# Kernel optimization log

Measured on AMD Instinct MI355X. Metric: run time of the kernel, lower is better.

Reference implementation:

```python
import jax, jax.numpy as jnp
import numpy as np


def setup_inputs() -> dict:
    key = jax.random.key(0)
    k1, k2, k3 = jax.random.split(key, 3)
    B, C, W, H, K = 8, 3, 512, 512, 13
    Wo, Ho = W - K + 1, H - K + 1
    return {
        "img": jax.random.normal(k1, (B, C, W, H), dtype=jnp.float32),
        "hori": jax.random.normal(k2, (B, K, Wo, Ho), dtype=jnp.float32),
        "vert": jax.random.normal(k3, (B, K, Wo, Ho), dtype=jnp.float32),
        "kernel_size": K,
    }


def reference(img, hori, vert, kernel_size):
    # out[b,c,i,j] = sum_{u,v} img[b,c,i+u,j+v] * vert[b,u,i,j] * hori[b,v,i,j]
    K = kernel_size
    B, C, W, H = img.shape
    Wo, Ho = W - K + 1, H - K + 1
    out = jnp.zeros((B, C, Wo, Ho), img.dtype)
    # Fixed small K x K loop over kernel taps; all pixel/batch dims vectorized.
    for v in range(K):
        h_v = hori[:, v][:, None]  # [B,1,Wo,Ho]
        acc = jnp.zeros((B, C, Wo, Ho), img.dtype)
        for u in range(K):
            acc = acc + img[:, :, u:u + Wo, v:v + Ho] * vert[:, u][:, None]
        out = out + acc * h_v
    return out
```

## Files before the change

kernel.cpp:

```cpp
#include <hip/hip_runtime.h>


#define KK 13
#define NB 8
#define NC 3
#define IW 512
#define IH 512
#define WO 500
#define HO 500
#define QROW 125
#define NT 384
#define NQ (KK * QROW)

typedef __attribute__((address_space(1))) const void g_void;
typedef __attribute__((address_space(3))) void l_void;

__global__ __launch_bounds__(NT) void sepconv_kernel(
    const float* __restrict__ img,
    const float* __restrict__ hori,
    const float* __restrict__ vert,
    float* __restrict__ out)
{
    __shared__ float4 s_vert[NQ];
    __shared__ float4 s_hori[NQ];

    const int tid = threadIdx.y * 128 + threadIdx.x;
    const int i = blockIdx.x;
    const int b = blockIdx.y;

    const size_t khw = (size_t)WO * HO;
    const size_t rs4 = khw / 4;
    const float4* vsrc = (const float4*)(vert + (size_t)b * KK * khw + (size_t)i * HO);
    const float4* hsrc = (const float4*)(hori + (size_t)b * KK * khw + (size_t)i * HO);

    #pragma unroll
    for (int f0 = 0; f0 < NQ; f0 += NT) {
        const int f = f0 + tid;
        if (f < NQ) {
            const unsigned u = (unsigned)f / QROW;
            const unsigned q = (unsigned)f - u * QROW;
            __builtin_amdgcn_global_load_lds(
                (g_void*)(vsrc + (size_t)u * rs4 + q),
                (l_void*)&s_vert[f], 16, 0, 0);
            __builtin_amdgcn_global_load_lds(
                (g_void*)(hsrc + (size_t)u * rs4 + q),
                (l_void*)&s_hori[f], 16, 0, 0);
        }
    }
    __syncthreads();

    const int tj = threadIdx.x;
    const int c  = threadIdx.y;
    if (tj >= QROW) return;
    const int j0 = tj * 4;

    const float* ibase = img + (((size_t)(b * NC + c) * IW) + i) * IH + j0;

    float tmp[4][KK];
    #pragma unroll
    for (int jq = 0; jq < 4; ++jq)
        #pragma unroll
        for (int v = 0; v < KK; ++v)
            tmp[jq][v] = 0.0f;

    float4 c0 = *(const float4*)(ibase + 0);
    float4 c1 = *(const float4*)(ibase + 4);
    float4 c2 = *(const float4*)(ibase + 8);
    float4 c3 = *(const float4*)(ibase + 12);

    #pragma unroll
    for (int u = 0; u < KK; ++u) {
        float4 n0, n1, n2, n3;
        if (u < KK - 1) {
            const float* rp = ibase + (size_t)(u + 1) * IH;
            n0 = *(const float4*)(rp + 0);
            n1 = *(const float4*)(rp + 4);
            n2 = *(const float4*)(rp + 8);
            n3 = *(const float4*)(rp + 12);
        }

        const float4 vt = s_vert[u * QROW + tj];

        float row[16];
        row[0]  = c0.x; row[1]  = c0.y; row[2]  = c0.z; row[3]  = c0.w;
        row[4]  = c1.x; row[5]  = c1.y; row[6]  = c1.z; row[7]  = c1.w;
        row[8]  = c2.x; row[9]  = c2.y; row[10] = c2.z; row[11] = c2.w;
        row[12] = c3.x; row[13] = c3.y; row[14] = c3.z; row[15] = c3.w;

        #pragma unroll
        for (int v = 0; v < KK; ++v) {
            tmp[0][v] += row[0 + v] * vt.x;
            tmp[1][v] += row[1 + v] * vt.y;
            tmp[2][v] += row[2 + v] * vt.z;
            tmp[3][v] += row[3 + v] * vt.w;
        }

        if (u < KK - 1) {
            c0 = n0; c1 = n1; c2 = n2; c3 = n3;
        }
    }

    float4 o = make_float4(0.f, 0.f, 0.f, 0.f);
    #pragma unroll
    for (int v = 0; v < KK; ++v) {
        const float4 hv = s_hori[v * QROW + tj];
        o.x += tmp[0][v] * hv.x;
        o.y += tmp[1][v] * hv.y;
        o.z += tmp[2][v] * hv.z;
        o.w += tmp[3][v] * hv.w;
    }

    float* op = out + (((size_t)(b * NC + c) * WO) + i) * HO + j0;
    *(float4*)op = o;
}

extern "C" void kernel_launch(void* const* d_in, const int* in_sizes, int n_in,
                              void* d_out, int out_size, void* d_ws, size_t ws_size,
                              hipStream_t stream) {
    const float* img  = (const float*)d_in[0];
    const float* hori = (const float*)d_in[1];
    const float* vert = (const float*)d_in[2];
    float* out = (float*)d_out;

    dim3 block(128, 3, 1);
    dim3 grid(WO, NB, 1);
    hipLaunchKernelGGL(sepconv_kernel, grid, block, 0, stream, img, hori, vert, out);
}
```

Measured before the change: 268.6 us.

## Process four output rows per block with double-buffered LDS weight staging

Each block now computes four consecutive output rows instead of one. While the current row is computed, the vert and hori weights for the next row are loaded asynchronously into a second LDS buffer, which hides global load latency and amortizes block launch cost. In exchange the grid is four times smaller, which lowers parallelism, LDS use doubles and lowers occupancy, and a barrier is added after each row.

```diff
diff --git a/kernel.cpp b/kernel.cpp
--- a/kernel.cpp
+++ b/kernel.cpp
@@ -10,10 +10,32 @@
 #define HO 500
 #define QROW 125
 #define NT 384
-#define NQ (KK * QROW)
+#define RPB 4
+#define NQ1 (KK * QROW)
+#define NQ2 (2 * NQ1)
 
 typedef __attribute__((address_space(1))) const void g_void;
 typedef __attribute__((address_space(3))) void l_void;
+
+__device__ __forceinline__ void stage_row(const float4* __restrict__ vrow,
+                                          const float4* __restrict__ hrow,
+                                          float4* dst, int tid, size_t rs4)
+{
+    #pragma unroll
+    for (int f0 = 0; f0 < NQ2; f0 += NT) {
+        const int f = f0 + tid;
+        if (f < NQ2) {
+            const bool is_v = (f < NQ1);
+            const int g = is_v ? f : f - NQ1;
+            const float4* base = is_v ? vrow : hrow;
+            const unsigned u = (unsigned)g / QROW;
+            const unsigned q = (unsigned)g - u * QROW;
+            __builtin_amdgcn_global_load_lds(
+                (g_void*)(base + (size_t)u * rs4 + q),
+                (l_void*)&dst[f], 16, 0, 0);
+        }
+    }
+}
 
 __global__ __launch_bounds__(NT) void sepconv_kernel(
     const float* __restrict__ img,
@@ -21,97 +43,99 @@
     const float* __restrict__ vert,
     float* __restrict__ out)
 {
-    __shared__ float4 s_vert[NQ];
-    __shared__ float4 s_hori[NQ];
+    __shared__ float4 s_w[2][NQ2];
 
     const int tid = threadIdx.y * 128 + threadIdx.x;
-    const int i = blockIdx.x;
-    const int b = blockIdx.y;
+    const int i0 = blockIdx.x * RPB;
+    const int b  = blockIdx.y;
 
     const size_t khw = (size_t)WO * HO;
     const size_t rs4 = khw / 4;
-    const float4* vsrc = (const float4*)(vert + (size_t)b * KK * khw + (size_t)i * HO);
-    const float4* hsrc = (const float4*)(hori + (size_t)b * KK * khw + (size_t)i * HO);
+    const float4* vb0 = (const float4*)(vert + (size_t)b * KK * khw);
+    const float4* hb0 = (const float4*)(hori + (size_t)b * KK * khw);
 
-    #pragma unroll
-    for (int f0 = 0; f0 < NQ; f0 += NT) {
-        const int f = f0 + tid;
-        if (f < NQ) {
-            const unsigned u = (unsigned)f / QROW;
-            const unsigned q = (unsigned)f - u * QROW;
-            __builtin_amdgcn_global_load_lds(
-                (g_void*)(vsrc + (size_t)u * rs4 + q),
-                (l_void*)&s_vert[f], 16, 0, 0);
-            __builtin_amdgcn_global_load_lds(
-                (g_void*)(hsrc + (size_t)u * rs4 + q),
-                (l_void*)&s_hori[f], 16, 0, 0);
-        }
-    }
+    stage_row(vb0 + (size_t)i0 * QROW, hb0 + (size_t)i0 * QROW,
+              s_w[0], tid, rs4);
     __syncthreads();
 
     const int tj = threadIdx.x;
     const int c  = threadIdx.y;
-    if (tj >= QROW) return;
+    const bool active = (tj < QROW);
     const int j0 = tj * 4;
 
-    const float* ibase = img + (((size_t)(b * NC + c) * IW) + i) * IH + j0;
+    for (int r = 0; r < RPB; ++r) {
+        if (r + 1 < RPB) {
+            const int in = i0 + r + 1;
+            stage_row(vb0 + (size_t)in * QROW, hb0 + (size_t)in * QROW,
+                      s_w[(r + 1) & 1], tid, rs4);
+        }
+        __builtin_amdgcn_sched_barrier(0);
 
-    float tmp[4][KK];
-    #pragma unroll
-    for (int jq = 0; jq < 4; ++jq)
-        #pragma unroll
-        for (int v = 0; v < KK; ++v)
-            tmp[jq][v] = 0.0f;
+        const float4* wb = s_w[r & 1];
+        if (active) {
+            const int i = i0 + r;
+            const float* ibase = img + (((size_t)(b * NC + c) * IW) + i) * IH + j0;
 
-    float4 c0 = *(const float4*)(ibase + 0);
-    float4 c1 = *(const float4*)(ibase + 4);
-    float4 c2 = *(const float4*)(ibase + 8);
-    float4 c3 = *(const float4*)(ibase + 12);
+            float tmp[4][KK];
+            #pragma unroll
+            for (int jq = 0; jq < 4; ++jq)
+                #pragma unroll
+                for (int v = 0; v < KK; ++v)
+                    tmp[jq][v] = 0.0f;
 
-    #pragma unroll
-    for (int u = 0; u < KK; ++u) {
-        float4 n0, n1, n2, n3;
-        if (u < KK - 1) {
-            const float* rp = ibase + (size_t)(u + 1) * IH;
-            n0 = *(const float4*)(rp + 0);
-            n1 = *(const float4*)(rp + 4);
-            n2 = *(const float4*)(rp + 8);
-            n3 = *(const float4*)(rp + 12);
+            float4 c0 = *(const float4*)(ibase + 0);
+            float4 c1 = *(const float4*)(ibase + 4);
+            float4 c2 = *(const float4*)(ibase + 8);
+            float4 c3 = *(const float4*)(ibase + 12);
+
+            #pragma unroll
+            for (int u = 0; u < KK; ++u) {
+                float4 n0, n1, n2, n3;
+                if (u < KK - 1) {
+                    const float* rp = ibase + (size_t)(u + 1) * IH;
+                    n0 = *(const float4*)(rp + 0);
+                    n1 = *(const float4*)(rp + 4);
+                    n2 = *(const float4*)(rp + 8);
+                    n3 = *(const float4*)(rp + 12);
+                }
+
+                const float4 vt = wb[u * QROW + tj];
+
+                float row[16];
+                row[0]  = c0.x; row[1]  = c0.y; row[2]  = c0.z; row[3]  = c0.w;
+                row[4]  = c1.x; row[5]  = c1.y; row[6]  = c1.z; row[7]  = c1.w;
+                row[8]  = c2.x; row[9]  = c2.y; row[10] = c2.z; row[11] = c2.w;
+                row[12] = c3.x; row[13] = c3.y; row[14] = c3.z; row[15] = c3.w;
+
+                #pragma unroll
+                for (int v = 0; v < KK; ++v) {
+                    tmp[0][v] += row[0 + v] * vt.x;
+                    tmp[1][v] += row[1 + v] * vt.y;
+                    tmp[2][v] += row[2 + v] * vt.z;
+                    tmp[3][v] += row[3 + v] * vt.w;
+                }
+
+                if (u < KK - 1) {
+                    c0 = n0; c1 = n1; c2 = n2; c3 = n3;
+                }
+            }
+
+            float4 o = make_float4(0.f, 0.f, 0.f, 0.f);
+            #pragma unroll
+            for (int v = 0; v < KK; ++v) {
+                const float4 hv = wb[NQ1 + v * QROW + tj];
+                o.x += tmp[0][v] * hv.x;
+                o.y += tmp[1][v] * hv.y;
+                o.z += tmp[2][v] * hv.z;
+                o.w += tmp[3][v] * hv.w;
+            }
+
+            float* op = out + (((size_t)(b * NC + c) * WO) + (size_t)(i0 + r)) * HO + j0;
+            *(float4*)op = o;
         }
 
-        const float4 vt = s_vert[u * QROW + tj];
-
-        float row[16];
-        row[0]  = c0.x; row[1]  = c0.y; row[2]  = c0.z; row[3]  = c0.w;
-        row[4]  = c1.x; row[5]  = c1.y; row[6]  = c1.z; row[7]  = c1.w;
-        row[8]  = c2.x; row[9]  = c2.y; row[10] = c2.z; row[11] = c2.w;
-        row[12] = c3.x; row[13] = c3.y; row[14] = c3.z; row[15] = c3.w;
-
-        #pragma unroll
-        for (int v = 0; v < KK; ++v) {
-            tmp[0][v] += row[0 + v] * vt.x;
-            tmp[1][v] += row[1 + v] * vt.y;
-            tmp[2][v] += row[2 + v] * vt.z;
-            tmp[3][v] += row[3 + v] * vt.w;
-        }
-
-        if (u < KK - 1) {
-            c0 = n0; c1 = n1; c2 = n2; c3 = n3;
-        }
+        __syncthreads();
     }
-
-    float4 o = make_float4(0.f, 0.f, 0.f, 0.f);
-    #pragma unroll
-    for (int v = 0; v < KK; ++v) {
-        const float4 hv = s_hori[v * QROW + tj];
-        o.x += tmp[0][v] * hv.x;
-        o.y += tmp[1][v] * hv.y;
-        o.z += tmp[2][v] * hv.z;
-        o.w += tmp[3][v] * hv.w;
-    }
-
-    float* op = out + (((size_t)(b * NC + c) * WO) + i) * HO + j0;
-    *(float4*)op = o;
 }
 
 extern "C" void kernel_launch(void* const* d_in, const int* in_sizes, int n_in,
@@ -123,6 +147,6 @@
     float* out = (float*)d_out;
 
     dim3 block(128, 3, 1);
-    dim3 grid(WO, NB, 1);
+    dim3 grid(WO / RPB, NB, 1);
     hipLaunchKernelGGL(sepconv_kernel, grid, block, 0, stream, img, hori, vert, out);
 }
```

New measurement: 536.2 us. +99.6%, slower.
